# Kernel tuning notes

Hardware: AMD Instinct MI355X
Metric: run time of the kernel (lower is better)

The kernel has to match this reference:

```python
import jax, jax.numpy as jnp
import numpy as np

N_NODES = 1_000_000
N_EDGES = 32_000_000
EPS_INIT = 100.0


def setup_inputs() -> dict:
    key = jax.random.key(0)
    ks = jax.random.split(key, 8)
    x = jax.random.normal(ks[0], (N_NODES, 1), dtype=jnp.float32)
    edge_index = jax.random.randint(ks[1], (2, N_EDGES), 0, N_NODES, dtype=jnp.int64)
    # MLP params: Linear(1,20) -> ReLU -> Linear(20,20) -> ReLU -> Linear(20,1)
    w1 = jax.random.normal(ks[2], (1, 20), dtype=jnp.float32) / np.sqrt(1.0)
    b1 = jnp.zeros((20,), dtype=jnp.float32)
    w2 = jax.random.normal(ks[3], (20, 20), dtype=jnp.float32) / np.sqrt(20.0)
    b2 = jnp.zeros((20,), dtype=jnp.float32)
    w3 = jax.random.normal(ks[4], (20, 1), dtype=jnp.float32) / np.sqrt(20.0)
    b3 = jnp.zeros((1,), dtype=jnp.float32)
    eps = jnp.asarray(EPS_INIT, dtype=jnp.float32)
    return {"x": x, "edge_index": edge_index, "eps": eps,
            "w1": w1, "b1": b1, "w2": w2, "b2": b2, "w3": w3, "b3": b3}


def reference(x, edge_index, eps, w1, b1, w2, b2, w3, b3):
    # GINConv: out = MLP((1 + eps) * x + sum_{j in N(i)} x_j)
    src, dst = edge_index[0], edge_index[1]
    # gather source features per edge, scatter-add to destination nodes
    agg = jax.ops.segment_sum(x[src], dst, num_segments=N_NODES)  # [N, 1]
    h = (1.0 + eps) * x + agg
    h = jax.nn.relu(h @ w1 + b1)   # [N, 20]
    h = jax.nn.relu(h @ w2 + b2)   # [N, 20]
    out = h @ w3 + b3              # [N, 1]
    return out
```

## Files before the change

### kernel.cpp

```cpp
#include <hip/hip_runtime.h>

#define N_NODES 1000000
#define N_EDGES 32000000

#define NB        256
#define TSC       1024
#define QPB       31250
#define NBKT      245
#define BKT_PAD   256
#define CAP       135168
#define RING      96
#define RSTRIDE   97
#define QSIZE     1024
#define TQ        1024
#define NT        ((QPB + TQ - 1) / TQ)

#define QSCALE    32768.0f
#define QINV      (1.0f / 32768.0f)

#define BINS_ELEMS  ((size_t)NBKT * CAP)
#define CNT_ELEMS   ((size_t)NB * BKT_PAD)
#define PAGG_ELEMS  ((size_t)NBKT * 2 * 4096)
#define WS_NEEDED   ((BINS_ELEMS + CNT_ELEMS + BKT_PAD + PAGG_ELEMS) * 4)

typedef int  iv4 __attribute__((ext_vector_type(4)));
typedef unsigned uv4 __attribute__((ext_vector_type(4)));


__global__ __launch_bounds__(TSC) void gin_count(const int* __restrict__ dst,
                                                 unsigned* __restrict__ cnt) {
    __shared__ unsigned h[BKT_PAD];
    int tid = threadIdx.x;
    if (tid < BKT_PAD) h[tid] = 0u;
    __syncthreads();
    int k = blockIdx.x;
    const iv4* q = reinterpret_cast<const iv4*>(dst) + (size_t)k * QPB;
    for (int base = 0; base < QPB; base += TSC * 4) {
        int i0 = base + tid, i1 = i0 + TSC, i2 = i1 + TSC, i3 = i2 + TSC;
        iv4 d0 = {0,0,0,0}, d1 = {0,0,0,0}, d2 = {0,0,0,0}, d3 = {0,0,0,0};
        bool v0 = i0 < QPB, v1 = i1 < QPB, v2 = i2 < QPB, v3 = i3 < QPB;
        if (v0) d0 = __builtin_nontemporal_load(&q[i0]);
        if (v1) d1 = __builtin_nontemporal_load(&q[i1]);
        if (v2) d2 = __builtin_nontemporal_load(&q[i2]);
        if (v3) d3 = __builtin_nontemporal_load(&q[i3]);
        if (v0) { atomicAdd(&h[d0.x >> 12], 1u); atomicAdd(&h[d0.y >> 12], 1u);
                  atomicAdd(&h[d0.z >> 12], 1u); atomicAdd(&h[d0.w >> 12], 1u); }
        if (v1) { atomicAdd(&h[d1.x >> 12], 1u); atomicAdd(&h[d1.y >> 12], 1u);
                  atomicAdd(&h[d1.z >> 12], 1u); atomicAdd(&h[d1.w >> 12], 1u); }
        if (v2) { atomicAdd(&h[d2.x >> 12], 1u); atomicAdd(&h[d2.y >> 12], 1u);
                  atomicAdd(&h[d2.z >> 12], 1u); atomicAdd(&h[d2.w >> 12], 1u); }
        if (v3) { atomicAdd(&h[d3.x >> 12], 1u); atomicAdd(&h[d3.y >> 12], 1u);
                  atomicAdd(&h[d3.z >> 12], 1u); atomicAdd(&h[d3.w >> 12], 1u); }
    }
    __syncthreads();
    if (tid < BKT_PAD) cnt[(size_t)k * BKT_PAD + tid] = h[tid];
}

__global__ void gin_scan(unsigned* __restrict__ cnt, unsigned* __restrict__ tot) {
    int gtid = blockIdx.x * blockDim.x + threadIdx.x;
    int b = gtid >> 6;
    int lane = gtid & 63;
    if (b >= BKT_PAD) return;
    unsigned running = 0;
    for (int base = 0; base < NB; base += 64) {
        int idx = base + lane;
        unsigned v = (idx < NB) ? cnt[(size_t)idx * BKT_PAD + b] : 0u;
        unsigned s = v;
        for (int d = 1; d < 64; d <<= 1) {
            unsigned u = __shfl_up(s, d);
            if (lane >= d) s += u;
        }
        unsigned excl = s - v;
        if (idx < NB) cnt[(size_t)idx * BKT_PAD + b] = running + excl;
        running += __shfl(s, 63);
    }
    if (lane == 0) tot[b] = running;
}

__global__ __launch_bounds__(TSC) void gin_scatter_fused(const int* __restrict__ src,
                                                         const int* __restrict__ dst,
                                                         const float* __restrict__ x,
                                                         const unsigned* __restrict__ cnt,
                                                         unsigned* __restrict__ bins) {
    __shared__ unsigned stage[BKT_PAD][RSTRIDE];
    __shared__ unsigned qv[2][TQ * 4];
    __shared__ unsigned stot[BKT_PAD];
    __shared__ unsigned sflt[BKT_PAD];
    __shared__ unsigned sbase[BKT_PAD];
    __shared__ unsigned queue[QSIZE];
    __shared__ unsigned qcount;

    int tid = threadIdx.x;
    int k = blockIdx.x;
    if (tid < BKT_PAD) {
        stot[tid] = 0u;
        sflt[tid] = 0u;
        sbase[tid] = cnt[(size_t)k * BKT_PAD + tid];
    }
    if (tid == 0) qcount = 0;

    const iv4* qs = reinterpret_cast<const iv4*>(src) + (size_t)k * QPB;
    const iv4* qd = reinterpret_cast<const iv4*>(dst) + (size_t)k * QPB;

#define QUANT(xx) ((unsigned)__float2int_rn((xx) * QSCALE) & 0xFFFFFu)

    bool isGW = tid >= 512;
    int g = tid & 511;
    int q0i = g, q1i = g + 512;

    iv4 a0 = {0,0,0,0}, a1 = {0,0,0,0};
    iv4 b0 = {0,0,0,0}, b1 = {0,0,0,0};

    if (isGW) {
        iv4 s0 = {0,0,0,0}, s1 = {0,0,0,0};
        if (q0i < QPB) s0 = __builtin_nontemporal_load(&qs[q0i]);
        if (q1i < QPB) s1 = __builtin_nontemporal_load(&qs[q1i]);
        int p0 = TQ + q0i, p1 = TQ + q1i;
        if (p0 < QPB) a0 = __builtin_nontemporal_load(&qs[p0]);
        if (p1 < QPB) a1 = __builtin_nontemporal_load(&qs[p1]);
        if (q0i < QPB) {
            qv[0][q0i * 4 + 0] = QUANT(x[s0.x]);
            qv[0][q0i * 4 + 1] = QUANT(x[s0.y]);
            qv[0][q0i * 4 + 2] = QUANT(x[s0.z]);
            qv[0][q0i * 4 + 3] = QUANT(x[s0.w]);
        }
        if (q1i < QPB) {
            qv[0][q1i * 4 + 0] = QUANT(x[s1.x]);
            qv[0][q1i * 4 + 1] = QUANT(x[s1.y]);
            qv[0][q1i * 4 + 2] = QUANT(x[s1.z]);
            qv[0][q1i * 4 + 3] = QUANT(x[s1.w]);
        }
    } else {
        if (q0i < QPB) a0 = __builtin_nontemporal_load(&qd[q0i]);
        if (q1i < QPB) a1 = __builtin_nontemporal_load(&qd[q1i]);
    }
    __syncthreads();

    for (int t = 0; t < NT; ++t) {
        int cur = t & 1, nxt = cur ^ 1;
        if (tid == 0) qcount = 0;
        if (isGW) {
            int p0 = (t + 2) * TQ + q0i, p1 = (t + 2) * TQ + q1i;
            b0 = (iv4){0,0,0,0}; b1 = (iv4){0,0,0,0};
            if (p0 < QPB) b0 = __builtin_nontemporal_load(&qs[p0]);
            if (p1 < QPB) b1 = __builtin_nontemporal_load(&qs[p1]);
            int u0 = (t + 1) * TQ + q0i, u1 = (t + 1) * TQ + q1i;
            if (u0 < QPB) {
                qv[nxt][q0i * 4 + 0] = QUANT(x[a0.x]);
                qv[nxt][q0i * 4 + 1] = QUANT(x[a0.y]);
                qv[nxt][q0i * 4 + 2] = QUANT(x[a0.z]);
                qv[nxt][q0i * 4 + 3] = QUANT(x[a0.w]);
            }
            if (u1 < QPB) {
                qv[nxt][q1i * 4 + 0] = QUANT(x[a1.x]);
                qv[nxt][q1i * 4 + 1] = QUANT(x[a1.y]);
                qv[nxt][q1i * 4 + 2] = QUANT(x[a1.z]);
                qv[nxt][q1i * 4 + 3] = QUANT(x[a1.w]);
            }
        } else {
            int p0 = (t + 1) * TQ + q0i, p1 = (t + 1) * TQ + q1i;
            b0 = (iv4){0,0,0,0}; b1 = (iv4){0,0,0,0};
            if (p0 < QPB) b0 = __builtin_nontemporal_load(&qd[p0]);
            if (p1 < QPB) b1 = __builtin_nontemporal_load(&qd[p1]);
            int u0 = t * TQ + q0i, u1 = t * TQ + q1i;
#define PUT(qq, dd) do {                                                     \
            unsigned b_ = (unsigned)(dd) >> 12;                              \
            unsigned p_ = atomicAdd(&stot[b_], 1u);                          \
            stage[b_][p_ % RING] =                                           \
                (((unsigned)(dd) & 4095u) << 20) | (qq);                     \
        } while (0)
            if (u0 < QPB) {
                PUT(qv[cur][q0i * 4 + 0], a0.x);
                PUT(qv[cur][q0i * 4 + 1], a0.y);
                PUT(qv[cur][q0i * 4 + 2], a0.z);
                PUT(qv[cur][q0i * 4 + 3], a0.w);
            }
            if (u1 < QPB) {
                PUT(qv[cur][q1i * 4 + 0], a1.x);
                PUT(qv[cur][q1i * 4 + 1], a1.y);
                PUT(qv[cur][q1i * 4 + 2], a1.z);
                PUT(qv[cur][q1i * 4 + 3], a1.w);
            }
#undef PUT
        }
        __syncthreads();
        if (tid < BKT_PAD) {
            unsigned T = stot[tid], F = sflt[tid];
            unsigned nch = (T - F) >> 5;
            if (nch) {
                unsigned off = atomicAdd(&qcount, nch);
                for (unsigned c = 0; c < nch; ++c)
                    queue[off + c] = ((unsigned)tid << 3) | c;
            }
        }
        __syncthreads();
        {
            unsigned C = qcount;
            unsigned lane = tid & 31;
            for (unsigned gg = tid >> 5; gg < C; gg += TSC / 32) {
                unsigned qe = queue[gg];
                unsigned b = qe >> 3, c = qe & 7;
                unsigned pos = sflt[b] + (c << 5) + lane;
                unsigned gp = sbase[b] + pos;
                if (gp < CAP)
                    __builtin_nontemporal_store(stage[b][pos % RING],
                                                &bins[(size_t)b * CAP + gp]);
            }
        }
        __syncthreads();
        if (tid < BKT_PAD) {
            unsigned T = stot[tid], F = sflt[tid];
            sflt[tid] = F + (((T - F) >> 5) << 5);
        }
        a0 = b0; a1 = b1;
    }
#undef QUANT
    __syncthreads();
    if (tid < BKT_PAD) {
        unsigned b = (unsigned)tid;
        unsigned T = stot[b];
        unsigned F = sflt[b];
        unsigned gbase = sbase[b];
        unsigned* gout = bins + (size_t)b * CAP;
        for (; F < T; ++F) {
            unsigned gp = gbase + F;
            if (gp < CAP) gout[gp] = stage[b][F % RING];
        }
    }
}

__global__ __launch_bounds__(1024) void gin_reduce(const unsigned* __restrict__ bins,
                                                   const unsigned* __restrict__ tot,
                                                   float* __restrict__ pagg) {
    __shared__ int acc[4096];
    int tid = threadIdx.x;
    int blk = blockIdx.x;
    int b = blk >> 1;
    int h = blk & 1;
    for (int i = tid; i < 4096; i += 1024) acc[i] = 0;
    __syncthreads();

    unsigned n = tot[b];
    if (n > CAP) n = CAP;
    const unsigned* bb = bins + (size_t)b * CAP;
    const uv4* bb4 = reinterpret_cast<const uv4*>(bb);
    unsigned nq = n >> 2;
    unsigned q_lo = h ? (nq >> 1) : 0;
    unsigned q_hi = h ? nq : (nq >> 1);

#define DEC(u) atomicAdd(&acc[(u) >> 20], ((int)((u) << 12)) >> 12)
    for (unsigned i = q_lo + tid; i < q_hi; i += 1024) {
        uv4 e = __builtin_nontemporal_load(&bb4[i]);
        DEC(e.x); DEC(e.y); DEC(e.z); DEC(e.w);
    }
    if (h) {
        for (unsigned j = (nq << 2) + tid; j < n; j += 1024) {
            unsigned e = __builtin_nontemporal_load(&bb[j]);
            DEC(e);
        }
    }
#undef DEC
    __syncthreads();

    float* po = pagg + (size_t)blk * 4096;
    for (int j = tid; j < 4096; j += 1024) po[j] = (float)acc[j] * QINV;
}

__global__ __launch_bounds__(512) void gin_combine_mlp(const float* __restrict__ pagg,
                               const float* __restrict__ x,
                               const float* __restrict__ eps,
                               const float* __restrict__ w1,
                               const float* __restrict__ b1,
                               const float* __restrict__ w2,
                               const float* __restrict__ b2,
                               const float* __restrict__ w3,
                               const float* __restrict__ b3,
                               float* __restrict__ out) {
    int i = blockIdx.x * blockDim.x + threadIdx.x;
    if (i >= N_NODES) return;
    int b = i >> 12;
    int j = i & 4095;
    float agg = pagg[(size_t)(b * 2) * 4096 + j] + pagg[(size_t)(b * 2 + 1) * 4096 + j];
    float h0 = (1.0f + eps[0]) * x[i] + agg;

    float h1[20];
#pragma unroll
    for (int jj = 0; jj < 20; ++jj)
        h1[jj] = fmaxf(fmaf(h0, w1[jj], b1[jj]), 0.0f);

    float o = b3[0];
#pragma unroll
    for (int kk = 0; kk < 20; ++kk) {
        float a = b2[kk];
#pragma unroll
        for (int jj = 0; jj < 20; ++jj)
            a = fmaf(h1[jj], w2[jj * 20 + kk], a);
        o = fmaf(fmaxf(a, 0.0f), w3[kk], o);
    }
    out[i] = o;
}

__global__ void gin_zero_kernel(float* __restrict__ agg, int n) {
    int i = blockIdx.x * blockDim.x + threadIdx.x;
    if (i < n) agg[i] = 0.0f;
}

__global__ void gin_scatter_kernel(const float* __restrict__ x,
                                   const int* __restrict__ src,
                                   const int* __restrict__ dst,
                                   float* __restrict__ agg) {
    int q = blockIdx.x * blockDim.x + threadIdx.x;
    int e = q * 4;
    if (e + 3 < N_EDGES) {
        int4 s = *reinterpret_cast<const int4*>(src + e);
        int4 d = *reinterpret_cast<const int4*>(dst + e);
        atomicAdd(&agg[d.x], x[s.x]);
        atomicAdd(&agg[d.y], x[s.y]);
        atomicAdd(&agg[d.z], x[s.z]);
        atomicAdd(&agg[d.w], x[s.w]);
    } else if (e < N_EDGES) {
        for (; e < N_EDGES; ++e) atomicAdd(&agg[dst[e]], x[src[e]]);
    }
}

__global__ void gin_mlp_kernel(const float* __restrict__ x,
                               const float* __restrict__ agg,
                               const float* __restrict__ eps,
                               const float* __restrict__ w1,
                               const float* __restrict__ b1,
                               const float* __restrict__ w2,
                               const float* __restrict__ b2,
                               const float* __restrict__ w3,
                               const float* __restrict__ b3,
                               float* __restrict__ out) {
    int i = blockIdx.x * blockDim.x + threadIdx.x;
    if (i >= N_NODES) return;
    float h0 = (1.0f + eps[0]) * x[i] + agg[i];
    float h1[20];
#pragma unroll
    for (int j = 0; j < 20; ++j) h1[j] = fmaxf(fmaf(h0, w1[j], b1[j]), 0.0f);
    float o = b3[0];
#pragma unroll
    for (int k = 0; k < 20; ++k) {
        float a = b2[k];
#pragma unroll
        for (int j = 0; j < 20; ++j) a = fmaf(h1[j], w2[j * 20 + k], a);
        o = fmaf(fmaxf(a, 0.0f), w3[k], o);
    }
    out[i] = o;
}

extern "C" void kernel_launch(void* const* d_in, const int* in_sizes, int n_in,
                              void* d_out, int out_size, void* d_ws, size_t ws_size,
                              hipStream_t stream) {
    const float* x    = (const float*)d_in[0];
    const int*   ei   = (const int*)  d_in[1];
    const float* eps  = (const float*)d_in[2];
    const float* w1   = (const float*)d_in[3];
    const float* b1   = (const float*)d_in[4];
    const float* w2   = (const float*)d_in[5];
    const float* b2   = (const float*)d_in[6];
    const float* w3   = (const float*)d_in[7];
    const float* b3   = (const float*)d_in[8];
    float* out = (float*)d_out;

    const int* src = ei;
    const int* dst = ei + N_EDGES;

    if (ws_size >= WS_NEEDED) {
        unsigned* bins = (unsigned*)d_ws;
        unsigned* cnt  = bins + BINS_ELEMS;
        unsigned* tot  = cnt + CNT_ELEMS;
        float*    pagg = (float*)(tot + BKT_PAD);

        gin_count<<<NB, TSC, 0, stream>>>(dst, cnt);
        {
            int blocks = (BKT_PAD * 64 + 255) / 256;
            gin_scan<<<blocks, 256, 0, stream>>>(cnt, tot);
        }
        gin_scatter_fused<<<NB, TSC, 0, stream>>>(src, dst, x, cnt, bins);
        gin_reduce<<<NBKT * 2, 1024, 0, stream>>>(bins, tot, pagg);
        gin_combine_mlp<<<(N_NODES + 511) / 512, 512, 0, stream>>>(pagg, x, eps,
                                                 w1, b1, w2, b2, w3, b3, out);
    } else {
        float* agg = (ws_size >= (size_t)N_NODES * sizeof(float)) ? (float*)d_ws : out;
        {
            int blocks = (N_NODES + 255) / 256;
            gin_zero_kernel<<<blocks, 256, 0, stream>>>(agg, N_NODES);
        }
        {
            int quads = N_EDGES / 4;
            int blocks = (quads + 255) / 256;
            gin_scatter_kernel<<<blocks, 256, 0, stream>>>(x, src, dst, agg);
        }
        {
            int blocks = (N_NODES + 255) / 256;
            gin_mlp_kernel<<<blocks, 256, 0, stream>>>(x, agg, eps, w1, b1, w2, b2,
                                                       w3, b3, out);
        }
    }
}
```

Measured before the change: 401.2 us.

## Replace count/scan prepass with global atomic bin allocation and fuse reduce with MLP

Drops the count and scan kernels, so the dst array is no longer read a second time. Each block now reserves space in every bucket with a global atomicAdd per 32-element chunk. The reduce kernel is merged with the MLP: one block per bucket accumulates in shared memory and evaluates the MLP directly, removing the pagg round trip and two launches. It also uses lighter LDS-only barriers and pads tail chunks with zeros so the reducer can read in aligned quads. The costs are global atomic contention, a larger bin capacity, and half as many reduce blocks as before.

```diff
diff --git a/kernel.cpp b/kernel.cpp
--- a/kernel.cpp
+++ b/kernel.cpp
@@ -8,7 +8,7 @@
 #define QPB       31250
 #define NBKT      245
 #define BKT_PAD   256
-#define CAP       135168
+#define CAP       143360
 #define RING      96
 #define RSTRIDE   97
 #define QSIZE     1024
@@ -19,74 +19,35 @@
 #define QINV      (1.0f / 32768.0f)
 
 #define BINS_ELEMS  ((size_t)NBKT * CAP)
-#define CNT_ELEMS   ((size_t)NB * BKT_PAD)
-#define PAGG_ELEMS  ((size_t)NBKT * 2 * 4096)
-#define WS_NEEDED   ((BINS_ELEMS + CNT_ELEMS + BKT_PAD + PAGG_ELEMS) * 4)
+#define WS_NEEDED   ((BINS_ELEMS + BKT_PAD) * 4)
 
 typedef int  iv4 __attribute__((ext_vector_type(4)));
 typedef unsigned uv4 __attribute__((ext_vector_type(4)));
 
-
-__global__ __launch_bounds__(TSC) void gin_count(const int* __restrict__ dst,
-                                                 unsigned* __restrict__ cnt) {
-    __shared__ unsigned h[BKT_PAD];
-    int tid = threadIdx.x;
-    if (tid < BKT_PAD) h[tid] = 0u;
-    __syncthreads();
-    int k = blockIdx.x;
-    const iv4* q = reinterpret_cast<const iv4*>(dst) + (size_t)k * QPB;
-    for (int base = 0; base < QPB; base += TSC * 4) {
-        int i0 = base + tid, i1 = i0 + TSC, i2 = i1 + TSC, i3 = i2 + TSC;
-        iv4 d0 = {0,0,0,0}, d1 = {0,0,0,0}, d2 = {0,0,0,0}, d3 = {0,0,0,0};
-        bool v0 = i0 < QPB, v1 = i1 < QPB, v2 = i2 < QPB, v3 = i3 < QPB;
-        if (v0) d0 = __builtin_nontemporal_load(&q[i0]);
-        if (v1) d1 = __builtin_nontemporal_load(&q[i1]);
-        if (v2) d2 = __builtin_nontemporal_load(&q[i2]);
-        if (v3) d3 = __builtin_nontemporal_load(&q[i3]);
-        if (v0) { atomicAdd(&h[d0.x >> 12], 1u); atomicAdd(&h[d0.y >> 12], 1u);
-                  atomicAdd(&h[d0.z >> 12], 1u); atomicAdd(&h[d0.w >> 12], 1u); }
-        if (v1) { atomicAdd(&h[d1.x >> 12], 1u); atomicAdd(&h[d1.y >> 12], 1u);
-                  atomicAdd(&h[d1.z >> 12], 1u); atomicAdd(&h[d1.w >> 12], 1u); }
-        if (v2) { atomicAdd(&h[d2.x >> 12], 1u); atomicAdd(&h[d2.y >> 12], 1u);
-                  atomicAdd(&h[d2.z >> 12], 1u); atomicAdd(&h[d2.w >> 12], 1u); }
-        if (v3) { atomicAdd(&h[d3.x >> 12], 1u); atomicAdd(&h[d3.y >> 12], 1u);
-                  atomicAdd(&h[d3.z >> 12], 1u); atomicAdd(&h[d3.w >> 12], 1u); }
-    }
-    __syncthreads();
-    if (tid < BKT_PAD) cnt[(size_t)k * BKT_PAD + tid] = h[tid];
-}
-
-__global__ void gin_scan(unsigned* __restrict__ cnt, unsigned* __restrict__ tot) {
-    int gtid = blockIdx.x * blockDim.x + threadIdx.x;
-    int b = gtid >> 6;
-    int lane = gtid & 63;
-    if (b >= BKT_PAD) return;
-    unsigned running = 0;
-    for (int base = 0; base < NB; base += 64) {
-        int idx = base + lane;
-        unsigned v = (idx < NB) ? cnt[(size_t)idx * BKT_PAD + b] : 0u;
-        unsigned s = v;
-        for (int d = 1; d < 64; d <<= 1) {
-            unsigned u = __shfl_up(s, d);
-            if (lane >= d) s += u;
-        }
-        unsigned excl = s - v;
-        if (idx < NB) cnt[(size_t)idx * BKT_PAD + b] = running + excl;
-        running += __shfl(s, 63);
-    }
-    if (lane == 0) tot[b] = running;
+#define BAR_LGKM() do {                                         \
+    __builtin_amdgcn_sched_barrier(0);                          \
+    asm volatile("s_waitcnt lgkmcnt(0)" ::: "memory");          \
+    __builtin_amdgcn_sched_barrier(0);                          \
+    __builtin_amdgcn_s_barrier();                               \
+    __builtin_amdgcn_sched_barrier(0);                          \
+} while (0)
+
+
+__global__ void gin_zero_galloc(unsigned* __restrict__ galloc) {
+    int i = threadIdx.x;
+    if (i < BKT_PAD) galloc[i] = 0u;
 }
 
 __global__ __launch_bounds__(TSC) void gin_scatter_fused(const int* __restrict__ src,
                                                          const int* __restrict__ dst,
                                                          const float* __restrict__ x,
-                                                         const unsigned* __restrict__ cnt,
+                                                         unsigned* __restrict__ galloc,
                                                          unsigned* __restrict__ bins) {
     __shared__ unsigned stage[BKT_PAD][RSTRIDE];
     __shared__ unsigned qv[2][TQ * 4];
     __shared__ unsigned stot[BKT_PAD];
     __shared__ unsigned sflt[BKT_PAD];
-    __shared__ unsigned sbase[BKT_PAD];
+    __shared__ unsigned gbase[BKT_PAD];
     __shared__ unsigned queue[QSIZE];
     __shared__ unsigned qcount;
 
@@ -95,7 +56,6 @@
     if (tid < BKT_PAD) {
         stot[tid] = 0u;
         sflt[tid] = 0u;
-        sbase[tid] = cnt[(size_t)k * BKT_PAD + tid];
     }
     if (tid == 0) qcount = 0;
 
@@ -183,17 +143,19 @@
             }
 #undef PUT
         }
-        __syncthreads();
+        BAR_LGKM();
         if (tid < BKT_PAD) {
             unsigned T = stot[tid], F = sflt[tid];
             unsigned nch = (T - F) >> 5;
             if (nch) {
                 unsigned off = atomicAdd(&qcount, nch);
+                unsigned gb = atomicAdd(&galloc[tid], nch << 5);
+                gbase[tid] = gb;
                 for (unsigned c = 0; c < nch; ++c)
                     queue[off + c] = ((unsigned)tid << 3) | c;
             }
         }
-        __syncthreads();
+        BAR_LGKM();
         {
             unsigned C = qcount;
             unsigned lane = tid & 31;
@@ -201,13 +163,13 @@
                 unsigned qe = queue[gg];
                 unsigned b = qe >> 3, c = qe & 7;
                 unsigned pos = sflt[b] + (c << 5) + lane;
-                unsigned gp = sbase[b] + pos;
+                unsigned gp = gbase[b] + (c << 5) + lane;
                 if (gp < CAP)
                     __builtin_nontemporal_store(stage[b][pos % RING],
                                                 &bins[(size_t)b * CAP + gp]);
             }
         }
-        __syncthreads();
+        BAR_LGKM();
         if (tid < BKT_PAD) {
             unsigned T = stot[tid], F = sflt[tid];
             sflt[tid] = F + (((T - F) >> 5) << 5);
@@ -218,55 +180,26 @@
     __syncthreads();
     if (tid < BKT_PAD) {
         unsigned b = (unsigned)tid;
-        unsigned T = stot[b];
-        unsigned F = sflt[b];
-        unsigned gbase = sbase[b];
-        unsigned* gout = bins + (size_t)b * CAP;
-        for (; F < T; ++F) {
-            unsigned gp = gbase + F;
-            if (gp < CAP) gout[gp] = stage[b][F % RING];
-        }
-    }
-}
-
-__global__ __launch_bounds__(1024) void gin_reduce(const unsigned* __restrict__ bins,
-                                                   const unsigned* __restrict__ tot,
-                                                   float* __restrict__ pagg) {
-    __shared__ int acc[4096];
-    int tid = threadIdx.x;
-    int blk = blockIdx.x;
-    int b = blk >> 1;
-    int h = blk & 1;
-    for (int i = tid; i < 4096; i += 1024) acc[i] = 0;
-    __syncthreads();
-
-    unsigned n = tot[b];
-    if (n > CAP) n = CAP;
-    const unsigned* bb = bins + (size_t)b * CAP;
-    const uv4* bb4 = reinterpret_cast<const uv4*>(bb);
-    unsigned nq = n >> 2;
-    unsigned q_lo = h ? (nq >> 1) : 0;
-    unsigned q_hi = h ? nq : (nq >> 1);
-
-#define DEC(u) atomicAdd(&acc[(u) >> 20], ((int)((u) << 12)) >> 12)
-    for (unsigned i = q_lo + tid; i < q_hi; i += 1024) {
-        uv4 e = __builtin_nontemporal_load(&bb4[i]);
-        DEC(e.x); DEC(e.y); DEC(e.z); DEC(e.w);
-    }
-    if (h) {
-        for (unsigned j = (nq << 2) + tid; j < n; j += 1024) {
-            unsigned e = __builtin_nontemporal_load(&bb[j]);
-            DEC(e);
-        }
-    }
-#undef DEC
-    __syncthreads();
-
-    float* po = pagg + (size_t)blk * 4096;
-    for (int j = tid; j < 4096; j += 1024) po[j] = (float)acc[j] * QINV;
-}
-
-__global__ __launch_bounds__(512) void gin_combine_mlp(const float* __restrict__ pagg,
+        unsigned T = stot[b], F = sflt[b];
+        unsigned rem = T - F;
+        if (rem) {
+            unsigned gb = atomicAdd(&galloc[b], 32u);
+            unsigned* gout = bins + (size_t)b * CAP;
+            unsigned i = 0;
+            for (; i < rem; ++i) {
+                unsigned gp = gb + i;
+                if (gp < CAP) gout[gp] = stage[b][(F + i) % RING];
+            }
+            for (; i < 32; ++i) {
+                unsigned gp = gb + i;
+                if (gp < CAP) gout[gp] = 0u;
+            }
+        }
+    }
+}
+
+__global__ __launch_bounds__(1024) void gin_reduce_mlp(const unsigned* __restrict__ bins,
+                               const unsigned* __restrict__ galloc,
                                const float* __restrict__ x,
                                const float* __restrict__ eps,
                                const float* __restrict__ w1,
@@ -276,28 +209,45 @@
                                const float* __restrict__ w3,
                                const float* __restrict__ b3,
                                float* __restrict__ out) {
-    int i = blockIdx.x * blockDim.x + threadIdx.x;
-    if (i >= N_NODES) return;
-    int b = i >> 12;
-    int j = i & 4095;
-    float agg = pagg[(size_t)(b * 2) * 4096 + j] + pagg[(size_t)(b * 2 + 1) * 4096 + j];
-    float h0 = (1.0f + eps[0]) * x[i] + agg;
-
-    float h1[20];
-#pragma unroll
-    for (int jj = 0; jj < 20; ++jj)
-        h1[jj] = fmaxf(fmaf(h0, w1[jj], b1[jj]), 0.0f);
-
-    float o = b3[0];
-#pragma unroll
-    for (int kk = 0; kk < 20; ++kk) {
-        float a = b2[kk];
+    __shared__ int acc[4096];
+    int tid = threadIdx.x;
+    int b = blockIdx.x;
+    for (int i = tid; i < 4096; i += 1024) acc[i] = 0;
+    __syncthreads();
+
+    unsigned n = galloc[b];
+    if (n > CAP) n = CAP;
+    const uv4* bb4 = reinterpret_cast<const uv4*>(bins + (size_t)b * CAP);
+    unsigned nq = n >> 2;
+#define DEC(u) atomicAdd(&acc[(u) >> 20], ((int)((u) << 12)) >> 12)
+    for (unsigned i = tid; i < nq; i += 1024) {
+        uv4 e = __builtin_nontemporal_load(&bb4[i]);
+        DEC(e.x); DEC(e.y); DEC(e.z); DEC(e.w);
+    }
+#undef DEC
+    __syncthreads();
+
+    float epsv = 1.0f + eps[0];
+    for (int j = tid; j < 4096; j += 1024) {
+        int node = (b << 12) + j;
+        if (node >= N_NODES) break;
+        float agg = (float)acc[j] * QINV;
+        float h0 = epsv * x[node] + agg;
+        float h1[20];
 #pragma unroll
         for (int jj = 0; jj < 20; ++jj)
-            a = fmaf(h1[jj], w2[jj * 20 + kk], a);
-        o = fmaf(fmaxf(a, 0.0f), w3[kk], o);
-    }
-    out[i] = o;
+            h1[jj] = fmaxf(fmaf(h0, w1[jj], b1[jj]), 0.0f);
+        float o = b3[0];
+#pragma unroll
+        for (int kk = 0; kk < 20; ++kk) {
+            float a = b2[kk];
+#pragma unroll
+            for (int jj = 0; jj < 20; ++jj)
+                a = fmaf(h1[jj], w2[jj * 20 + kk], a);
+            o = fmaf(fmaxf(a, 0.0f), w3[kk], o);
+        }
+        out[node] = o;
+    }
 }
 
 __global__ void gin_zero_kernel(float* __restrict__ agg, int n) {
@@ -368,20 +318,13 @@
     const int* dst = ei + N_EDGES;
 
     if (ws_size >= WS_NEEDED) {
-        unsigned* bins = (unsigned*)d_ws;
-        unsigned* cnt  = bins + BINS_ELEMS;
-        unsigned* tot  = cnt + CNT_ELEMS;
-        float*    pagg = (float*)(tot + BKT_PAD);
-
-        gin_count<<<NB, TSC, 0, stream>>>(dst, cnt);
-        {
-            int blocks = (BKT_PAD * 64 + 255) / 256;
-            gin_scan<<<blocks, 256, 0, stream>>>(cnt, tot);
-        }
-        gin_scatter_fused<<<NB, TSC, 0, stream>>>(src, dst, x, cnt, bins);
-        gin_reduce<<<NBKT * 2, 1024, 0, stream>>>(bins, tot, pagg);
-        gin_combine_mlp<<<(N_NODES + 511) / 512, 512, 0, stream>>>(pagg, x, eps,
-                                                 w1, b1, w2, b2, w3, b3, out);
+        unsigned* bins   = (unsigned*)d_ws;
+        unsigned* galloc = bins + BINS_ELEMS;
+
+        gin_zero_galloc<<<1, 256, 0, stream>>>(galloc);
+        gin_scatter_fused<<<NB, TSC, 0, stream>>>(src, dst, x, galloc, bins);
+        gin_reduce_mlp<<<NBKT, 1024, 0, stream>>>(bins, galloc, x, eps,
+                                                  w1, b1, w2, b2, w3, b3, out);
     } else {
         float* agg = (ws_size >= (size_t)N_NODES * sizeof(float)) ? (float*)d_ws : out;
         {
```

After: 341.1 us (median of 2 runs). 1.18x faster.
